# Performance work log

Hardware: AMD Instinct MI355X
Metric: run time of the kernel (lower is better)

## Reference

```python
import jax, jax.numpy as jnp
import numpy as np

B, T, D = 32, 2048, 256
H, OUT = 256, 256


def setup_inputs() -> dict:
    key = jax.random.key(0)
    ks = jax.random.split(key, 7)
    s = 0.05
    x = jax.random.normal(ks[0], (B, T, D), dtype=jnp.float32)
    # TF GRUCell params: gate kernel [D+H, 2H] (r,u), candidate kernel [D+H, H]
    Wg = jax.random.normal(ks[1], (D + H, 2 * H), dtype=jnp.float32) * s
    bg = jnp.ones((2 * H,), dtype=jnp.float32)  # TF GRUCell gate bias init = 1.0
    Wc = jax.random.normal(ks[2], (D + H, H), dtype=jnp.float32) * s
    bc = jnp.zeros((H,), dtype=jnp.float32)
    Wp = jax.random.normal(ks[3], (H, OUT), dtype=jnp.float32) * s
    bp = jnp.zeros((OUT,), dtype=jnp.float32)
    return {"x": x, "Wg": Wg, "bg": bg, "Wc": Wc, "bc": bc, "Wp": Wp, "bp": bp}


def _gru_scan(x, Wg, bg, Wc, bc):
    # x: [B, T, D] -> outputs [B, T, H]
    xT = jnp.swapaxes(x, 0, 1)  # [T, B, D]
    h0 = jnp.zeros((x.shape[0], Wc.shape[1]), dtype=x.dtype)

    def step(h, x_t):
        xh = jnp.concatenate([x_t, h], axis=-1)            # [B, D+H]
        ru = jax.nn.sigmoid(xh @ Wg + bg)                  # [B, 2H]
        r, u = jnp.split(ru, 2, axis=-1)
        xc = jnp.concatenate([x_t, r * h], axis=-1)        # [B, D+H]
        c = jnp.tanh(xc @ Wc + bc)
        h_new = u * h + (1.0 - u) * c
        return h_new, h_new

    _, outs = jax.lax.scan(step, h0, xT)                   # [T, B, H]
    return jnp.swapaxes(outs, 0, 1)                        # [B, T, H]


def reference(x, Wg, bg, Wc, bc, Wp, bp):
    rnn_outputs = _gru_scan(x, Wg, bg, Wc, bc)             # [B, T, H]
    # map_fn(linear+sigmoid) over batch == dense on last dim
    return jax.nn.sigmoid(rnn_outputs @ Wp + bp)           # [B, T, OUT]
```

## Files before the change

kernel.cpp:

```cpp
#include <hip/hip_runtime.h>

typedef unsigned int u32;
typedef unsigned long long u64;
typedef float    f4  __attribute__((ext_vector_type(4)));
typedef _Float16 h2v __attribute__((ext_vector_type(2)));

#define B_ 32
#define T_ 2048
#define D_ 256
#define H_ 256
#define G_ 512


__device__ __forceinline__ float fsigmoid(float x){
  return 1.f / (1.f + __expf(-x));
}
__device__ __forceinline__ float ftanh(float x){
  float a = fabsf(x);
  float e = __expf(2.f * a);
  float t = 1.f - 2.f / (e + 1.f);
  return copysignf(t, x);
}
__device__ __forceinline__ u32 pack2(float a, float b){
  h2v p = {(_Float16)a, (_Float16)b};
  return __builtin_bit_cast(u32, p);
}
__device__ __forceinline__ u64 tag_pack(float v, u32 tag){
  return ((u64)__builtin_bit_cast(u32, v) << 32) | (u64)tag;
}
__device__ __forceinline__ float tag_val(u64 x){
  return __builtin_bit_cast(float, (u32)(x >> 32));
}

__global__ __launch_bounds__(256) void pack_w(
    const float* __restrict__ Wg, const float* __restrict__ Wc,
    float* __restrict__ wgp)
{
  int idx = blockIdx.x * 256 + threadIdx.x;
  int j  = idx / 98304;
  int r2 = idx - j * 98304;
  int r = r2 >> 9;
  int t = r2 & 511;
  float v;
  if (r < 128){
    v = Wg[(size_t)(256 + 128*j + r) * G_ + t];
  } else {
    int rr = r - 128;
    int w = t >> 6, l = t & 63;
    int g = w >> 2, a = w & 3, lh = (l >> 5) & 1;
    int c2 = 32*a + (l & 31);
    int kr = 128*g + 64*lh + rr;
    v = Wc[(size_t)(256 + kr) * H_ + 128*j + c2];
  }
  wgp[idx] = v;
}

__global__ __launch_bounds__(256) void input_proj(
    const float* __restrict__ X, const float* __restrict__ Wg, const float* __restrict__ bg,
    const float* __restrict__ Wc, const float* __restrict__ bc,
    float* __restrict__ gx, float* __restrict__ cx)
{
  __shared__ __align__(16) float At[16][64];
  __shared__ __align__(16) float Bt[16][64];
  const int t  = threadIdx.x;
  const int m0 = blockIdx.x*64, n0 = blockIdx.y*64;
  const int tm = (t & 15)*4, tn = (t >> 4)*4;
  const int lm = t >> 2,  lk = (t & 3)*4;
  const int bk = t >> 4,  bn = (t & 15)*4;
  const float* bsrc; int bld;
  if (n0 < G_) { bsrc = Wg + n0; bld = G_; } else { bsrc = Wc + (n0 - G_); bld = H_; }
  float acc[4][4] = {};
  for (int kc = 0; kc < D_; kc += 16){
    __syncthreads();
    f4 a4 = *(const f4*)&X[(size_t)(m0+lm)*D_ + kc + lk];
    f4 b4 = *(const f4*)&bsrc[(size_t)(kc+bk)*bld + bn];
    At[lk+0][lm] = a4.x; At[lk+1][lm] = a4.y; At[lk+2][lm] = a4.z; At[lk+3][lm] = a4.w;
    *(f4*)&Bt[bk][bn] = b4;
    __syncthreads();
#pragma unroll
    for (int k = 0; k < 16; ++k){
      f4 av = *(const f4*)&At[k][tm];
      f4 bv = *(const f4*)&Bt[k][tn];
#pragma unroll
      for (int i = 0; i < 4; ++i){
        acc[i][0] = fmaf(av[i], bv[0], acc[i][0]);
        acc[i][1] = fmaf(av[i], bv[1], acc[i][1]);
        acc[i][2] = fmaf(av[i], bv[2], acc[i][2]);
        acc[i][3] = fmaf(av[i], bv[3], acc[i][3]);
      }
    }
  }
  if (n0 < G_){
    f4 bb = { bg[n0+tn], bg[n0+tn+1], bg[n0+tn+2], bg[n0+tn+3] };
#pragma unroll
    for (int i = 0; i < 4; ++i){
      f4 v = { acc[i][0]+bb.x, acc[i][1]+bb.y, acc[i][2]+bb.z, acc[i][3]+bb.w };
      *(f4*)&gx[(size_t)(m0+tm+i)*G_ + n0 + tn] = v;
    }
  } else {
    int nn = n0 - G_;
    f4 bb = { bc[nn+tn], bc[nn+tn+1], bc[nn+tn+2], bc[nn+tn+3] };
#pragma unroll
    for (int i = 0; i < 4; ++i){
      f4 v = { acc[i][0]+bb.x, acc[i][1]+bb.y, acc[i][2]+bb.z, acc[i][3]+bb.w };
      *(f4*)&cx[(size_t)(m0+tm+i)*H_ + nn + tn] = v;
    }
  }
}

__global__ __launch_bounds__(512)
__attribute__((amdgpu_waves_per_eu(2, 2)))
void gru_pair(
    const float* __restrict__ gx,
    const float* __restrict__ cx,
    const float* __restrict__ wgp,
    u64* __restrict__ pay,
    unsigned short* __restrict__ hseq)
{
  __shared__ __align__(16) float h32[128];
  __shared__ __align__(16) float rh[256];
  __shared__ __align__(16) float ug[128];
  __shared__ __align__(16) float part2[4][128];

  const int tid = threadIdx.x;
  const int w = tid >> 6, l = tid & 63;
  const int b = blockIdx.x & 31;
  const int j = blockIdx.x >> 5;

  const bool is_r   = (tid < 256);
  const int  su     = (tid - 256) >> 7;
  const bool is_myu = (tid >= 256) && (su == j);
  const int  i_u    = tid - 256 - 128*j;
  const int  i_pu   = tid - 256 - 128*(1-j);
  const bool h_from_pay = is_r && (((tid >> 7) & 1) != j);
  const int  hcol   = tid & 127;

  const int g2 = w >> 2, aw = w & 3, lh = (l >> 5) & 1;
  const int c2 = 32*aw + (l & 31);
  const int q2 = 2*g2 + lh;
  const int kb = 128*g2 + 64*lh;

  const float* wbase = wgp + (size_t)j * 98304;
  float wg[128];
#pragma unroll
  for (int r = 0; r < 128; ++r) wg[r] = wbase[(size_t)r*512 + tid];
  float wc[64];
#pragma unroll
  for (int r = 0; r < 64; ++r) wc[r] = wbase[(size_t)(128+r)*512 + tid];
#pragma unroll
  for (int r = 0; r < 128; ++r) asm volatile("" : "+v"(wg[r]));
#pragma unroll
  for (int r = 0; r < 64; ++r) asm volatile("" : "+v"(wc[r]));

  if (tid < 128) h32[tid] = 0.f;
  __syncthreads();

  const float* gxb = gx + (size_t)b * T_ * G_;
  const float* cxb = cx + (size_t)b * T_ * H_ + 128*j;
  unsigned short* hb = hseq + (size_t)b * T_ * H_ + 128*j;

  u64* own0 = pay + ((size_t)(b*2 + j)*2    ) * 512;
  u64* own1 = own0 + 512;
  u64* oth0 = pay + ((size_t)(b*2 + (1-j))*2) * 512;
  u64* oth1 = oth0 + 512;

  for (int t = 0; t < T_; ++t){
    const u32 tag = (u32)(t + 1);
    u64* own = (t & 1) ? own1 : own0;
    u64* oth = (t & 1) ? oth1 : oth0;

    if (is_myu)
      __hip_atomic_store(own + 384 + i_u, tag_pack(h32[i_u], tag),
                         __ATOMIC_RELAXED, __HIP_MEMORY_SCOPE_AGENT);

    float g = gxb[(size_t)t * G_ + tid];
    f4 c4 = {0.f, 0.f, 0.f, 0.f};
    if (tid < 32) c4 = *(const f4*)(cxb + (size_t)t * H_ + 4*tid);

    float a0 = 0.f, a1 = 0.f, a2 = 0.f, a3 = 0.f;
#pragma unroll
    for (int kc = 0; kc < 128; kc += 16){
      f4 h0 = *(const f4*)&h32[kc + 0];
      f4 h1 = *(const f4*)&h32[kc + 4];
      f4 h2 = *(const f4*)&h32[kc + 8];
      f4 h3 = *(const f4*)&h32[kc + 12];
      a0 = fmaf(wg[kc+ 0], h0.x, a0); a1 = fmaf(wg[kc+ 1], h0.y, a1);
      a2 = fmaf(wg[kc+ 2], h0.z, a2); a3 = fmaf(wg[kc+ 3], h0.w, a3);
      a0 = fmaf(wg[kc+ 4], h1.x, a0); a1 = fmaf(wg[kc+ 5], h1.y, a1);
      a2 = fmaf(wg[kc+ 6], h1.z, a2); a3 = fmaf(wg[kc+ 7], h1.w, a3);
      a0 = fmaf(wg[kc+ 8], h2.x, a0); a1 = fmaf(wg[kc+ 9], h2.y, a1);
      a2 = fmaf(wg[kc+10], h2.z, a2); a3 = fmaf(wg[kc+11], h2.w, a3);
      a0 = fmaf(wg[kc+12], h3.x, a0); a1 = fmaf(wg[kc+13], h3.y, a1);
      a2 = fmaf(wg[kc+14], h3.z, a2); a3 = fmaf(wg[kc+15], h3.w, a3);
    }
    float acc = (a0 + a1) + (a2 + a3);

    if (is_r)
      __hip_atomic_store(own + tid, tag_pack(acc, tag),
                         __ATOMIC_RELAXED, __HIP_MEMORY_SCOPE_AGENT);
    else if (!is_myu)
      __hip_atomic_store(own + 256 + i_pu, tag_pack(acc, tag),
                         __ATOMIC_RELAXED, __HIP_MEMORY_SCOPE_AGENT);

    asm volatile("" ::: "memory");

    if (is_r){
      if (h_from_pay){
        u64 vp, vh;
        for (;;){
          vp = __hip_atomic_load(oth + tid,        __ATOMIC_RELAXED, __HIP_MEMORY_SCOPE_AGENT);
          vh = __hip_atomic_load(oth + 384 + hcol, __ATOMIC_RELAXED, __HIP_MEMORY_SCOPE_AGENT);
          if (((u32)vp == tag) & ((u32)vh == tag)) break;
        }
        float pre = acc + tag_val(vp) + g;
        rh[tid] = fsigmoid(pre) * tag_val(vh);
      } else {
        u64 vp;
        for (;;){
          vp = __hip_atomic_load(oth + tid, __ATOMIC_RELAXED, __HIP_MEMORY_SCOPE_AGENT);
          if ((u32)vp == tag) break;
        }
        float pre = acc + tag_val(vp) + g;
        rh[tid] = fsigmoid(pre) * h32[hcol];
      }
    } else if (is_myu){
      u64 vp;
      for (;;){
        vp = __hip_atomic_load(oth + 256 + i_u, __ATOMIC_RELAXED, __HIP_MEMORY_SCOPE_AGENT);
        if ((u32)vp == tag) break;
      }
      float pre = acc + tag_val(vp) + g;
      ug[i_u] = fsigmoid(pre);
    }
    __syncthreads();

    float s0 = 0.f, s1 = 0.f, s2 = 0.f, s3 = 0.f;
#pragma unroll
    for (int kc = 0; kc < 64; kc += 16){
      f4 r0 = *(const f4*)&rh[kb + kc + 0];
      f4 r1 = *(const f4*)&rh[kb + kc + 4];
      f4 r2 = *(const f4*)&rh[kb + kc + 8];
      f4 r3 = *(const f4*)&rh[kb + kc + 12];
      s0 = fmaf(wc[kc+ 0], r0.x, s0); s1 = fmaf(wc[kc+ 1], r0.y, s1);
      s2 = fmaf(wc[kc+ 2], r0.z, s2); s3 = fmaf(wc[kc+ 3], r0.w, s3);
      s0 = fmaf(wc[kc+ 4], r1.x, s0); s1 = fmaf(wc[kc+ 5], r1.y, s1);
      s2 = fmaf(wc[kc+ 6], r1.z, s2); s3 = fmaf(wc[kc+ 7], r1.w, s3);
      s0 = fmaf(wc[kc+ 8], r2.x, s0); s1 = fmaf(wc[kc+ 9], r2.y, s1);
      s2 = fmaf(wc[kc+10], r2.z, s2); s3 = fmaf(wc[kc+11], r2.w, s3);
      s0 = fmaf(wc[kc+12], r3.x, s0); s1 = fmaf(wc[kc+13], r3.y, s1);
      s2 = fmaf(wc[kc+14], r3.z, s2); s3 = fmaf(wc[kc+15], r3.w, s3);
    }
    part2[q2][c2] = (s0 + s1) + (s2 + s3);
    __syncthreads();

    if (tid < 32){
      f4 s = *(const f4*)&part2[0][4*tid];
      s += *(const f4*)&part2[1][4*tid];
      s += *(const f4*)&part2[2][4*tid];
      s += *(const f4*)&part2[3][4*tid];
      s += c4;
      f4 cv;
      cv.x = ftanh(s.x); cv.y = ftanh(s.y);
      cv.z = ftanh(s.z); cv.w = ftanh(s.w);
      f4 uv = *(const f4*)&ug[4*tid];
      f4 hv = *(const f4*)&h32[4*tid];
      f4 one = {1.f, 1.f, 1.f, 1.f};
      f4 hn = uv*hv + (one - uv)*cv;
      *(f4*)&h32[4*tid] = hn;
      uint2 pk;
      pk.x = pack2(hn.x, hn.y);
      pk.y = pack2(hn.z, hn.w);
      *(uint2*)(hb + (size_t)t*H_ + 4*tid) = pk;
    }
    __syncthreads();
  }
}

__global__ __launch_bounds__(256) void out_proj(
    const unsigned short* __restrict__ hs, const float* __restrict__ Wp,
    const float* __restrict__ bp, float* __restrict__ out)
{
  __shared__ __align__(16) float At[16][64];
  __shared__ __align__(16) float Bt[16][64];
  const int t  = threadIdx.x;
  const int m0 = blockIdx.x*64, n0 = blockIdx.y*64;
  const int tm = (t & 15)*4, tn = (t >> 4)*4;
  const int lm = t >> 2,  lk = (t & 3)*4;
  const int bk = t >> 4,  bn = (t & 15)*4;
  float acc[4][4] = {};
  for (int kc = 0; kc < H_; kc += 16){
    __syncthreads();
    uint2 a2 = *(const uint2*)(hs + (size_t)(m0+lm)*H_ + kc + lk);
    f4  b4 = *(const f4*)&Wp[(size_t)(kc+bk)*256 + n0 + bn];
    h2v a0 = __builtin_bit_cast(h2v, a2.x), a1 = __builtin_bit_cast(h2v, a2.y);
    At[lk+0][lm] = (float)a0.x; At[lk+1][lm] = (float)a0.y;
    At[lk+2][lm] = (float)a1.x; At[lk+3][lm] = (float)a1.y;
    *(f4*)&Bt[bk][bn] = b4;
    __syncthreads();
#pragma unroll
    for (int k = 0; k < 16; ++k){
      f4 av = *(const f4*)&At[k][tm];
      f4 bv = *(const f4*)&Bt[k][tn];
#pragma unroll
      for (int i = 0; i < 4; ++i){
        acc[i][0] = fmaf(av[i], bv[0], acc[i][0]);
        acc[i][1] = fmaf(av[i], bv[1], acc[i][1]);
        acc[i][2] = fmaf(av[i], bv[2], acc[i][2]);
        acc[i][3] = fmaf(av[i], bv[3], acc[i][3]);
      }
    }
  }
  float b0=bp[n0+tn], b1=bp[n0+tn+1], b2=bp[n0+tn+2], b3=bp[n0+tn+3];
#pragma unroll
  for (int i = 0; i < 4; ++i){
    f4 r;
    r.x = fsigmoid(acc[i][0]+b0); r.y = fsigmoid(acc[i][1]+b1);
    r.z = fsigmoid(acc[i][2]+b2); r.w = fsigmoid(acc[i][3]+b3);
    *(f4*)&out[(size_t)(m0+tm+i)*256 + n0 + tn] = r;
  }
}

extern "C" void kernel_launch(void* const* d_in, const int* in_sizes, int n_in,
                              void* d_out, int out_size, void* d_ws, size_t ws_size,
                              hipStream_t stream)
{
  const float* x  = (const float*)d_in[0];
  const float* Wg = (const float*)d_in[1];
  const float* bg = (const float*)d_in[2];
  const float* Wc = (const float*)d_in[3];
  const float* bc = (const float*)d_in[4];
  const float* Wp = (const float*)d_in[5];
  const float* bp = (const float*)d_in[6];
  float* out = (float*)d_out;

  char* ws = (char*)d_ws;
  float* Gx = (float*)(ws);
  float* Cx = (float*)(ws + (size_t)134217728);
  unsigned short* Hs = (unsigned short*)(ws + (size_t)201326592);
  float* wgp = (float*)(ws + (size_t)234881024);
  u64* pay = (u64*)(ws + (size_t)235667456);

  pack_w<<<768, 256, 0, stream>>>(Wg, Wc, wgp);
  input_proj<<<dim3(1024, 12), 256, 0, stream>>>(x, Wg, bg, Wc, bc, Gx, Cx);
  gru_pair<<<64, 512, 0, stream>>>(Gx, Cx, wgp, pay, Hs);
  out_proj<<<dim3(1024, 4), 256, 0, stream>>>(Hs, Wp, bp, out);
}
```

Baseline: 5.735 ms.

## Process two batch rows per GRU block pair and publish h at step end

Each block pair now handles two batch sequences at once, halving the grid from 64 to 32 blocks. The recurrent GEMV and candidate GEMV loop over both sequences while reusing the register-resident weights. The goal is to spread per-step latency, barriers and cross-block handshakes over twice the work. The h half-state is now published to the partner block right after the update, for the next step, instead of at the start of the next step. The cost is longer per-step critical paths, twice the payload buffer size, and fewer CUs in use.

Result: slower. 6.218 ms (+8.4%).

```diff
diff --git a/kernel.cpp b/kernel.cpp
--- a/kernel.cpp
+++ b/kernel.cpp
@@ -117,15 +117,15 @@
     u64* __restrict__ pay,
     unsigned short* __restrict__ hseq)
 {
-  __shared__ __align__(16) float h32[128];
-  __shared__ __align__(16) float rh[256];
-  __shared__ __align__(16) float ug[128];
-  __shared__ __align__(16) float part2[4][128];
+  __shared__ __align__(16) float h32[2][128];
+  __shared__ __align__(16) float rh[2][256];
+  __shared__ __align__(16) float ug[2][128];
+  __shared__ __align__(16) float part2[2][4][128];
 
   const int tid = threadIdx.x;
   const int w = tid >> 6, l = tid & 63;
-  const int b = blockIdx.x & 31;
-  const int j = blockIdx.x >> 5;
+  const int p = blockIdx.x & 15;
+  const int j = blockIdx.x >> 4;
 
   const bool is_r   = (tid < 256);
   const int  su     = (tid - 256) >> 7;
@@ -152,125 +152,146 @@
 #pragma unroll
   for (int r = 0; r < 64; ++r) asm volatile("" : "+v"(wc[r]));
 
-  if (tid < 128) h32[tid] = 0.f;
+  if (tid < 256) h32[tid >> 7][tid & 127] = 0.f;
   __syncthreads();
 
-  const float* gxb = gx + (size_t)b * T_ * G_;
-  const float* cxb = cx + (size_t)b * T_ * H_ + 128*j;
-  unsigned short* hb = hseq + (size_t)b * T_ * H_ + 128*j;
-
-  u64* own0 = pay + ((size_t)(b*2 + j)*2    ) * 512;
-  u64* own1 = own0 + 512;
-  u64* oth0 = pay + ((size_t)(b*2 + (1-j))*2) * 512;
-  u64* oth1 = oth0 + 512;
+  const float* gxb0 = gx + (size_t)(2*p + 0) * T_ * G_;
+  const float* gxb1 = gx + (size_t)(2*p + 1) * T_ * G_;
+  const float* cxk  = cx + (size_t)(2*p + ((tid >> 5) & 1)) * T_ * H_ + 128*j;
+  unsigned short* hbk = hseq + (size_t)(2*p + ((tid >> 5) & 1)) * T_ * H_ + 128*j;
+
+  u64* own_base = pay + (size_t)(p*2 + j)     * 2048;
+  u64* oth_base = pay + (size_t)(p*2 + (1-j)) * 2048;
+
+  if (tid < 128){
+    __hip_atomic_store(own_base +   0 + 384 + tid, tag_pack(0.f, 1u),
+                       __ATOMIC_RELAXED, __HIP_MEMORY_SCOPE_AGENT);
+    __hip_atomic_store(own_base + 512 + 384 + tid, tag_pack(0.f, 1u),
+                       __ATOMIC_RELAXED, __HIP_MEMORY_SCOPE_AGENT);
+  }
 
   for (int t = 0; t < T_; ++t){
     const u32 tag = (u32)(t + 1);
-    u64* own = (t & 1) ? own1 : own0;
-    u64* oth = (t & 1) ? oth1 : oth0;
-
-    if (is_myu)
-      __hip_atomic_store(own + 384 + i_u, tag_pack(h32[i_u], tag),
-                         __ATOMIC_RELAXED, __HIP_MEMORY_SCOPE_AGENT);
-
-    float g = gxb[(size_t)t * G_ + tid];
+    u64* ownp = own_base + (size_t)(t & 1) * 1024;
+    u64* othp = oth_base + (size_t)(t & 1) * 1024;
+
+    float g0 = gxb0[(size_t)t * G_ + tid];
+    float g1 = gxb1[(size_t)t * G_ + tid];
     f4 c4 = {0.f, 0.f, 0.f, 0.f};
-    if (tid < 32) c4 = *(const f4*)(cxb + (size_t)t * H_ + 4*tid);
-
-    float a0 = 0.f, a1 = 0.f, a2 = 0.f, a3 = 0.f;
-#pragma unroll
-    for (int kc = 0; kc < 128; kc += 16){
-      f4 h0 = *(const f4*)&h32[kc + 0];
-      f4 h1 = *(const f4*)&h32[kc + 4];
-      f4 h2 = *(const f4*)&h32[kc + 8];
-      f4 h3 = *(const f4*)&h32[kc + 12];
-      a0 = fmaf(wg[kc+ 0], h0.x, a0); a1 = fmaf(wg[kc+ 1], h0.y, a1);
-      a2 = fmaf(wg[kc+ 2], h0.z, a2); a3 = fmaf(wg[kc+ 3], h0.w, a3);
-      a0 = fmaf(wg[kc+ 4], h1.x, a0); a1 = fmaf(wg[kc+ 5], h1.y, a1);
-      a2 = fmaf(wg[kc+ 6], h1.z, a2); a3 = fmaf(wg[kc+ 7], h1.w, a3);
-      a0 = fmaf(wg[kc+ 8], h2.x, a0); a1 = fmaf(wg[kc+ 9], h2.y, a1);
-      a2 = fmaf(wg[kc+10], h2.z, a2); a3 = fmaf(wg[kc+11], h2.w, a3);
-      a0 = fmaf(wg[kc+12], h3.x, a0); a1 = fmaf(wg[kc+13], h3.y, a1);
-      a2 = fmaf(wg[kc+14], h3.z, a2); a3 = fmaf(wg[kc+15], h3.w, a3);
-    }
-    float acc = (a0 + a1) + (a2 + a3);
-
-    if (is_r)
-      __hip_atomic_store(own + tid, tag_pack(acc, tag),
-                         __ATOMIC_RELAXED, __HIP_MEMORY_SCOPE_AGENT);
-    else if (!is_myu)
-      __hip_atomic_store(own + 256 + i_pu, tag_pack(acc, tag),
-                         __ATOMIC_RELAXED, __HIP_MEMORY_SCOPE_AGENT);
+    if (tid < 64) c4 = *(const f4*)(cxk + (size_t)t * H_ + 4*(tid & 31));
+
+    float accs[2];
+#pragma unroll
+    for (int k = 0; k < 2; ++k){
+      float a0 = 0.f, a1 = 0.f, a2 = 0.f, a3 = 0.f;
+#pragma unroll
+      for (int kc = 0; kc < 128; kc += 16){
+        f4 h0 = *(const f4*)&h32[k][kc + 0];
+        f4 h1 = *(const f4*)&h32[k][kc + 4];
+        f4 h2 = *(const f4*)&h32[k][kc + 8];
+        f4 h3 = *(const f4*)&h32[k][kc + 12];
+        a0 = fmaf(wg[kc+ 0], h0.x, a0); a1 = fmaf(wg[kc+ 1], h0.y, a1);
+        a2 = fmaf(wg[kc+ 2], h0.z, a2); a3 = fmaf(wg[kc+ 3], h0.w, a3);
+        a0 = fmaf(wg[kc+ 4], h1.x, a0); a1 = fmaf(wg[kc+ 5], h1.y, a1);
+        a2 = fmaf(wg[kc+ 6], h1.z, a2); a3 = fmaf(wg[kc+ 7], h1.w, a3);
+        a0 = fmaf(wg[kc+ 8], h2.x, a0); a1 = fmaf(wg[kc+ 9], h2.y, a1);
+        a2 = fmaf(wg[kc+10], h2.z, a2); a3 = fmaf(wg[kc+11], h2.w, a3);
+        a0 = fmaf(wg[kc+12], h3.x, a0); a1 = fmaf(wg[kc+13], h3.y, a1);
+        a2 = fmaf(wg[kc+14], h3.z, a2); a3 = fmaf(wg[kc+15], h3.w, a3);
+      }
+      accs[k] = (a0 + a1) + (a2 + a3);
+      if (is_r)
+        __hip_atomic_store(ownp + k*512 + tid, tag_pack(accs[k], tag),
+                           __ATOMIC_RELAXED, __HIP_MEMORY_SCOPE_AGENT);
+      else if (!is_myu)
+        __hip_atomic_store(ownp + k*512 + 256 + i_pu, tag_pack(accs[k], tag),
+                           __ATOMIC_RELAXED, __HIP_MEMORY_SCOPE_AGENT);
+    }
 
     asm volatile("" ::: "memory");
 
-    if (is_r){
-      if (h_from_pay){
-        u64 vp, vh;
-        for (;;){
-          vp = __hip_atomic_load(oth + tid,        __ATOMIC_RELAXED, __HIP_MEMORY_SCOPE_AGENT);
-          vh = __hip_atomic_load(oth + 384 + hcol, __ATOMIC_RELAXED, __HIP_MEMORY_SCOPE_AGENT);
-          if (((u32)vp == tag) & ((u32)vh == tag)) break;
+#pragma unroll
+    for (int k = 0; k < 2; ++k){
+      const float g = k ? g1 : g0;
+      u64* othk = othp + k*512;
+      if (is_r){
+        if (h_from_pay){
+          u64 vp, vh;
+          for (;;){
+            vp = __hip_atomic_load(othk + tid,        __ATOMIC_RELAXED, __HIP_MEMORY_SCOPE_AGENT);
+            vh = __hip_atomic_load(othk + 384 + hcol, __ATOMIC_RELAXED, __HIP_MEMORY_SCOPE_AGENT);
+            if (((u32)vp == tag) & ((u32)vh == tag)) break;
+          }
+          float pre = accs[k] + tag_val(vp) + g;
+          rh[k][tid] = fsigmoid(pre) * tag_val(vh);
+        } else {
+          u64 vp;
+          for (;;){
+            vp = __hip_atomic_load(othk + tid, __ATOMIC_RELAXED, __HIP_MEMORY_SCOPE_AGENT);
+            if ((u32)vp == tag) break;
+          }
+          float pre = accs[k] + tag_val(vp) + g;
+          rh[k][tid] = fsigmoid(pre) * h32[k][hcol];
         }
-        float pre = acc + tag_val(vp) + g;
-        rh[tid] = fsigmoid(pre) * tag_val(vh);
-      } else {
+      } else if (is_myu){
         u64 vp;
         for (;;){
-          vp = __hip_atomic_load(oth + tid, __ATOMIC_RELAXED, __HIP_MEMORY_SCOPE_AGENT);
+          vp = __hip_atomic_load(othk + 256 + i_u, __ATOMIC_RELAXED, __HIP_MEMORY_SCOPE_AGENT);
           if ((u32)vp == tag) break;
         }
-        float pre = acc + tag_val(vp) + g;
-        rh[tid] = fsigmoid(pre) * h32[hcol];
-      }
-    } else if (is_myu){
-      u64 vp;
-      for (;;){
-        vp = __hip_atomic_load(oth + 256 + i_u, __ATOMIC_RELAXED, __HIP_MEMORY_SCOPE_AGENT);
-        if ((u32)vp == tag) break;
-      }
-      float pre = acc + tag_val(vp) + g;
-      ug[i_u] = fsigmoid(pre);
-    }
-    __syncthreads();
-
-    float s0 = 0.f, s1 = 0.f, s2 = 0.f, s3 = 0.f;
-#pragma unroll
-    for (int kc = 0; kc < 64; kc += 16){
-      f4 r0 = *(const f4*)&rh[kb + kc + 0];
-      f4 r1 = *(const f4*)&rh[kb + kc + 4];
-      f4 r2 = *(const f4*)&rh[kb + kc + 8];
-      f4 r3 = *(const f4*)&rh[kb + kc + 12];
-      s0 = fmaf(wc[kc+ 0], r0.x, s0); s1 = fmaf(wc[kc+ 1], r0.y, s1);
-      s2 = fmaf(wc[kc+ 2], r0.z, s2); s3 = fmaf(wc[kc+ 3], r0.w, s3);
-      s0 = fmaf(wc[kc+ 4], r1.x, s0); s1 = fmaf(wc[kc+ 5], r1.y, s1);
-      s2 = fmaf(wc[kc+ 6], r1.z, s2); s3 = fmaf(wc[kc+ 7], r1.w, s3);
-      s0 = fmaf(wc[kc+ 8], r2.x, s0); s1 = fmaf(wc[kc+ 9], r2.y, s1);
-      s2 = fmaf(wc[kc+10], r2.z, s2); s3 = fmaf(wc[kc+11], r2.w, s3);
-      s0 = fmaf(wc[kc+12], r3.x, s0); s1 = fmaf(wc[kc+13], r3.y, s1);
-      s2 = fmaf(wc[kc+14], r3.z, s2); s3 = fmaf(wc[kc+15], r3.w, s3);
-    }
-    part2[q2][c2] = (s0 + s1) + (s2 + s3);
-    __syncthreads();
-
-    if (tid < 32){
-      f4 s = *(const f4*)&part2[0][4*tid];
-      s += *(const f4*)&part2[1][4*tid];
-      s += *(const f4*)&part2[2][4*tid];
-      s += *(const f4*)&part2[3][4*tid];
+        float pre = accs[k] + tag_val(vp) + g;
+        ug[k][i_u] = fsigmoid(pre);
+      }
+    }
+    __syncthreads();
+
+#pragma unroll
+    for (int k = 0; k < 2; ++k){
+      float s0 = 0.f, s1 = 0.f, s2 = 0.f, s3 = 0.f;
+#pragma unroll
+      for (int kc = 0; kc < 64; kc += 16){
+        f4 r0 = *(const f4*)&rh[k][kb + kc + 0];
+        f4 r1 = *(const f4*)&rh[k][kb + kc + 4];
+        f4 r2 = *(const f4*)&rh[k][kb + kc + 8];
+        f4 r3 = *(const f4*)&rh[k][kb + kc + 12];
+        s0 = fmaf(wc[kc+ 0], r0.x, s0); s1 = fmaf(wc[kc+ 1], r0.y, s1);
+        s2 = fmaf(wc[kc+ 2], r0.z, s2); s3 = fmaf(wc[kc+ 3], r0.w, s3);
+        s0 = fmaf(wc[kc+ 4], r1.x, s0); s1 = fmaf(wc[kc+ 5], r1.y, s1);
+        s2 = fmaf(wc[kc+ 6], r1.z, s2); s3 = fmaf(wc[kc+ 7], r1.w, s3);
+        s0 = fmaf(wc[kc+ 8], r2.x, s0); s1 = fmaf(wc[kc+ 9], r2.y, s1);
+        s2 = fmaf(wc[kc+10], r2.z, s2); s3 = fmaf(wc[kc+11], r2.w, s3);
+        s0 = fmaf(wc[kc+12], r3.x, s0); s1 = fmaf(wc[kc+13], r3.y, s1);
+        s2 = fmaf(wc[kc+14], r3.z, s2); s3 = fmaf(wc[kc+15], r3.w, s3);
+      }
+      part2[k][q2][c2] = (s0 + s1) + (s2 + s3);
+    }
+    __syncthreads();
+
+    if (tid < 64){
+      const int k  = (tid >> 5) & 1;
+      const int ii = tid & 31;
+      f4 s = *(const f4*)&part2[k][0][4*ii];
+      s += *(const f4*)&part2[k][1][4*ii];
+      s += *(const f4*)&part2[k][2][4*ii];
+      s += *(const f4*)&part2[k][3][4*ii];
       s += c4;
       f4 cv;
       cv.x = ftanh(s.x); cv.y = ftanh(s.y);
       cv.z = ftanh(s.z); cv.w = ftanh(s.w);
-      f4 uv = *(const f4*)&ug[4*tid];
-      f4 hv = *(const f4*)&h32[4*tid];
+      f4 uv = *(const f4*)&ug[k][4*ii];
+      f4 hv = *(const f4*)&h32[k][4*ii];
       f4 one = {1.f, 1.f, 1.f, 1.f};
       f4 hn = uv*hv + (one - uv)*cv;
-      *(f4*)&h32[4*tid] = hn;
+      *(f4*)&h32[k][4*ii] = hn;
+      u64* ow = own_base + (size_t)((t+1) & 1) * 1024 + (size_t)k*512 + 384 + 4*ii;
+      __hip_atomic_store(ow + 0, tag_pack(hn.x, tag + 1), __ATOMIC_RELAXED, __HIP_MEMORY_SCOPE_AGENT);
+      __hip_atomic_store(ow + 1, tag_pack(hn.y, tag + 1), __ATOMIC_RELAXED, __HIP_MEMORY_SCOPE_AGENT);
+      __hip_atomic_store(ow + 2, tag_pack(hn.z, tag + 1), __ATOMIC_RELAXED, __HIP_MEMORY_SCOPE_AGENT);
+      __hip_atomic_store(ow + 3, tag_pack(hn.w, tag + 1), __ATOMIC_RELAXED, __HIP_MEMORY_SCOPE_AGENT);
       uint2 pk;
       pk.x = pack2(hn.x, hn.y);
       pk.y = pack2(hn.z, hn.w);
-      *(uint2*)(hb + (size_t)t*H_ + 4*tid) = pk;
+      *(uint2*)(hbk + (size_t)t*H_ + 4*ii) = pk;
     }
     __syncthreads();
   }
@@ -342,6 +363,6 @@
 
   pack_w<<<768, 256, 0, stream>>>(Wg, Wc, wgp);
   input_proj<<<dim3(1024, 12), 256, 0, stream>>>(x, Wg, bg, Wc, bc, Gx, Cx);
-  gru_pair<<<64, 512, 0, stream>>>(Gx, Cx, wgp, pay, Hs);
+  gru_pair<<<32, 512, 0, stream>>>(Gx, Cx, wgp, pay, Hs);
   out_proj<<<dim3(1024, 4), 256, 0, stream>>>(Hs, Wp, bp, out);
 }
```
